# Performance work log

Measured on AMD Instinct MI355X. Metric: run time of the kernel, lower is better.

The kernel has to match this reference:

```python
import jax, jax.numpy as jnp
import numpy as np
from jax import lax

EPS = 1e-5

# sign binarization with straight-through-estimator gradient (identity),
# matching the .data-swap trick in BinarizeConv2d/BinarizeLinear.
@jax.custom_vjp
def ste_sign(x):
    return jnp.sign(x)

def _ste_fwd(x):
    return jnp.sign(x), None

def _ste_bwd(_, g):
    return (g,)

ste_sign.defvjp(_ste_fwd, _ste_bwd)


def conv3x3(x, w):
    # weight is binarized inside the layer; padding=1, stride=1, no bias
    return lax.conv_general_dilated(
        x, ste_sign(w), window_strides=(1, 1), padding=((1, 1), (1, 1)),
        dimension_numbers=('NCHW', 'OIHW', 'NCHW'))


def mp2(x):
    return lax.reduce_window(x, -jnp.inf, lax.max, (1, 1, 2, 2), (1, 1, 2, 2), 'VALID')


def bn2d(x, gamma, beta):
    # training-mode BatchNorm2d: batch statistics over (N, H, W)
    mu = jnp.mean(x, axis=(0, 2, 3), keepdims=True)
    var = jnp.var(x, axis=(0, 2, 3), keepdims=True)
    xn = (x - mu) * lax.rsqrt(var + EPS)
    return xn * gamma[None, :, None, None] + beta[None, :, None, None]


def bn1d(x, gamma=None, beta=None):
    mu = jnp.mean(x, axis=0, keepdims=True)
    var = jnp.var(x, axis=0, keepdims=True)
    xn = (x - mu) * lax.rsqrt(var + EPS)
    if gamma is None:
        return xn
    return xn * gamma[None, :] + beta[None, :]


def hardtanh(x):
    return jnp.clip(x, -1.0, 1.0)


def setup_inputs() -> dict:
    key = jax.random.key(0)
    ks = jax.random.split(key, 16)
    def w(k, shape):
        return jax.random.normal(k, shape, jnp.float32) * 0.1
    d = {'x': jax.random.normal(ks[0], (512, 3, 32, 32), jnp.float32)}
    convs = [(64, 3), (64, 64), (128, 64), (128, 128), (256, 128), (256, 256)]
    for i, (co, ci) in enumerate(convs):
        d[f'w{i+1}'] = w(ks[1 + i], (co, ci, 3, 3))
        d[f'g{i+1}'] = jnp.ones((co,), jnp.float32)
        d[f'b{i+1}'] = jnp.zeros((co,), jnp.float32)
    d['wf1'] = w(ks[7], (512, 256 * 4 * 4))
    d['gf1'] = jnp.ones((512,), jnp.float32)
    d['bf1'] = jnp.zeros((512,), jnp.float32)
    d['wf2'] = w(ks[8], (512, 512))
    d['gf2'] = jnp.ones((512,), jnp.float32)
    d['bf2'] = jnp.zeros((512,), jnp.float32)
    d['wf3'] = w(ks[9], (10, 512))
    return d


def reference(x, w1, g1, b1, w2, g2, b2, w3, g3, b3, w4, g4, b4,
              w5, g5, b5, w6, g6, b6, wf1, gf1, bf1, wf2, gf2, bf2, wf3):
    # block 1: first conv sees raw 3-channel input (not binarized)
    h = hardtanh(bn2d(conv3x3(x, w1), g1, b1))
    h = hardtanh(bn2d(mp2(conv3x3(ste_sign(h), w2)), g2, b2))
    # block 2
    h = hardtanh(bn2d(conv3x3(ste_sign(h), w3), g3, b3))
    h = hardtanh(bn2d(mp2(conv3x3(ste_sign(h), w4)), g4, b4))
    # block 3
    h = hardtanh(bn2d(conv3x3(ste_sign(h), w5), g5, b5))
    h = hardtanh(bn2d(mp2(conv3x3(ste_sign(h), w6)), g6, b6))
    # classifier (all linear inputs binarized: feature dim != 784)
    h = h.reshape(-1, 256 * 4 * 4)
    h = hardtanh(bn1d(ste_sign(h) @ ste_sign(wf1).T, gf1, bf1))
    h = hardtanh(bn1d(ste_sign(h) @ ste_sign(wf2).T, gf2, bf2))
    h = bn1d(ste_sign(h) @ ste_sign(wf3).T)  # affine=False
    return jax.nn.log_softmax(h, axis=-1)
```

## Files before the change

kernel.cpp:

```cpp
#include <hip/hip_runtime.h>
#include <stdint.h>
#include <math.h>


typedef unsigned long long u64;

__device__ __forceinline__ void flag_and_wave(u64* flag, u64 nz) {
    nz &= __shfl_xor(nz, 1);
    nz &= __shfl_xor(nz, 2);
    nz &= __shfl_xor(nz, 4);
    nz &= __shfl_xor(nz, 8);
    nz &= __shfl_xor(nz, 16);
    nz &= __shfl_xor(nz, 32);
    if ((threadIdx.x & 63) == 0) atomicAnd(flag, nz);
}

__global__ void kflag_init(u64* __restrict__ f) {
    int i = threadIdx.x;
    if (i < 16) f[i] = ~0ull;
}

__global__ void kw1t(const float* __restrict__ w1, float* __restrict__ wt) {
    int i = blockIdx.x * 64 + threadIdx.x;
    if (i >= 64 * 27) return;
    int co = i / 27, k = i % 27;
    float v = w1[i];
    wt[k * 64 + co] = (v > 0.f) ? 1.f : ((v < 0.f) ? -1.f : 0.f);
}

__global__ __launch_bounds__(256) void k1_conv_allv(const float* __restrict__ x,
                                                    const float* __restrict__ wt,
                                                    float* __restrict__ out) {
    int gid = blockIdx.x * 256 + threadIdx.x;
    int n = gid >> 8, hw0 = (gid & 255) * 4;
    int y = hw0 >> 5, x0 = hw0 & 31;
    const float* ip = x + (size_t)n * 3 * 1024;
    for (int c0 = 0; c0 < 64; c0 += 16) {
        float4 a[16];
#pragma unroll
        for (int c = 0; c < 16; ++c) a[c] = make_float4(0.f, 0.f, 0.f, 0.f);
        for (int ky = 0; ky < 3; ++ky) {
            int yy = y + ky - 1;
            bool rowok = (unsigned)yy < 32u;
            float win[3][6];
#pragma unroll
            for (int ci = 0; ci < 3; ++ci)
#pragma unroll
                for (int j = 0; j < 6; ++j) {
                    int cc = x0 - 1 + j;
                    bool ok = rowok && ((unsigned)cc < 32u);
                    win[ci][j] = ok ? ip[ci * 1024 + yy * 32 + cc] : 0.f;
                }
#pragma unroll
            for (int kx = 0; kx < 3; ++kx)
#pragma unroll
                for (int ci = 0; ci < 3; ++ci) {
                    const float* wrow = wt + (ci * 9 + ky * 3 + kx) * 64 + c0;
                    float s0 = win[ci][kx], s1 = win[ci][kx + 1];
                    float s2 = win[ci][kx + 2], s3 = win[ci][kx + 3];
#pragma unroll
                    for (int c = 0; c < 16; ++c) {
                        float wv = wrow[c];
                        a[c].x = fmaf(wv, s0, a[c].x);
                        a[c].y = fmaf(wv, s1, a[c].y);
                        a[c].z = fmaf(wv, s2, a[c].z);
                        a[c].w = fmaf(wv, s3, a[c].w);
                    }
                }
        }
#pragma unroll
        for (int c = 0; c < 16; ++c)
            *(float4*)(out + ((size_t)n * 64 + c0 + c) * 1024 + hw0) = a[c];
    }
}

__global__ void k1_statsA(const float* __restrict__ v, double* __restrict__ Sp,
                          double* __restrict__ S2p, int N) {
    int c = blockIdx.x;
    int slot = blockIdx.y * 64 + threadIdx.x;
    double s = 0.0, s2 = 0.0;
    int K = N * 4;
    const float* vp = v + (size_t)c * 1024 + slot;
    int k0 = 0;
    for (; k0 + 32 <= K; k0 += 32) {
        const float* p0 = vp + (size_t)(k0 >> 2) * 65536;
        float buf[32];
#pragma unroll
        for (int j = 0; j < 32; ++j)
            buf[j] = p0[(size_t)(j >> 2) * 65536 + (j & 3) * 256];
#pragma unroll
        for (int j = 0; j < 32; ++j) {
            double t = (double)buf[j];
            s += t; s2 += t * t;
        }
    }
    for (; k0 < K; ++k0) {
        int m = slot + k0 * 256;
        double t = (double)v[((size_t)(m >> 10) * 64 + c) * 1024 + (m & 1023)];
        s += t; s2 += t * t;
    }
    Sp[c * 256 + slot] = s; S2p[c * 256 + slot] = s2;
}

__global__ void k1_statsB(const double* __restrict__ Sp, const double* __restrict__ S2p,
                          float* __restrict__ muF, float* __restrict__ rF, int N) {
    int c = blockIdx.x;
    __shared__ double sh[256], sh2[256];
    sh[threadIdx.x]  = Sp[c * 256 + threadIdx.x];
    sh2[threadIdx.x] = S2p[c * 256 + threadIdx.x];
    __syncthreads();
    for (int o = 128; o > 0; o >>= 1) {
        if ((int)threadIdx.x < o) { sh[threadIdx.x] += sh[threadIdx.x + o]; sh2[threadIdx.x] += sh2[threadIdx.x + o]; }
        __syncthreads();
    }
    if (threadIdx.x == 0) {
        int M = N * 1024;
        double mean = sh[0] / M;
        double var  = sh2[0] / M - mean * mean;
        if (var < 0.0) var = 0.0;
        muF[c] = (float)mean;
        rF[c]  = 1.0f / sqrtf((float)var + 1e-5f);
    }
}

__global__ void k1_signpack(const float* __restrict__ v, const float* __restrict__ muF,
                            const float* __restrict__ rF, const float* __restrict__ g,
                            const float* __restrict__ b, u64* __restrict__ B,
                            u64* __restrict__ NZ, u64* __restrict__ aflag) {
    int gid = blockIdx.x * 64 + threadIdx.x;
    int n = gid >> 8, hw0 = (gid & 255) * 4;
    const float* vp = v + ((size_t)n * 64) * 1024 + hw0;
    u64 bb0 = 0, bb1 = 0, bb2 = 0, bb3 = 0;
    u64 nz0 = 0, nz1 = 0, nz2 = 0, nz3 = 0;
    for (int c0 = 0; c0 < 64; c0 += 16) {
        float4 buf[16];
#pragma unroll
        for (int j = 0; j < 16; ++j)
            buf[j] = *(const float4*)(vp + (size_t)(c0 + j) * 1024);
#pragma unroll
        for (int j = 0; j < 16; ++j) {
            int c = c0 + j;
            float mc = muF[c], rc = rF[c], gc = g[c], bc = b[c];
            float d0 = buf[j].x - mc; float t0 = (d0 * rc) * gc + bc;
            float d1 = buf[j].y - mc; float t1 = (d1 * rc) * gc + bc;
            float d2 = buf[j].z - mc; float t2 = (d2 * rc) * gc + bc;
            float d3 = buf[j].w - mc; float t3 = (d3 * rc) * gc + bc;
            bb0 |= (u64)(t0 > 0.f) << c;  nz0 |= (u64)(t0 != 0.f) << c;
            bb1 |= (u64)(t1 > 0.f) << c;  nz1 |= (u64)(t1 != 0.f) << c;
            bb2 |= (u64)(t2 > 0.f) << c;  nz2 |= (u64)(t2 != 0.f) << c;
            bb3 |= (u64)(t3 > 0.f) << c;  nz3 |= (u64)(t3 != 0.f) << c;
        }
    }
    size_t o = (size_t)n * 1024 + hw0;
    B[o]     = bb0; B[o + 1]  = bb1; B[o + 2]  = bb2; B[o + 3]  = bb3;
    NZ[o]    = nz0; NZ[o + 1] = nz1; NZ[o + 2] = nz2; NZ[o + 3] = nz3;
    flag_and_wave(aflag, nz0 & nz1 & nz2 & nz3);
}

__global__ void k1_conv(const float* __restrict__ x, const float* __restrict__ w1,
                        float* __restrict__ out, int grp) {
    int hw = blockIdx.x * 64 + threadIdx.x;
    int cg = blockIdx.y;
    int n  = blockIdx.z;
    int co = grp * 8 + cg;
    int y = hw >> 5, x0 = hw & 31;
    const float* ip0 = x + ((size_t)n * 3 + 0) * 1024;
    const float* ip1 = x + ((size_t)n * 3 + 1) * 1024;
    const float* ip2 = x + ((size_t)n * 3 + 2) * 1024;
    const float* wp  = w1 + (size_t)co * 27;
    float acc = 0.f;
    for (int ky = 0; ky < 3; ++ky) {
        int yy = y + ky - 1;
        if (yy < 0 || yy > 31) continue;
        for (int kx = 0; kx < 3; ++kx) {
            int xc = x0 + kx - 1;
            if (xc < 0 || xc > 31) continue;
            int sp = yy * 32 + xc;
            int wk = ky * 3 + kx;
            float w0 = wp[wk], w1v = wp[9 + wk], w2 = wp[18 + wk];
            acc += (w0  > 0.f) ? ip0[sp] : ((w0  < 0.f) ? -ip0[sp] : 0.f);
            acc += (w1v > 0.f) ? ip1[sp] : ((w1v < 0.f) ? -ip1[sp] : 0.f);
            acc += (w2  > 0.f) ? ip2[sp] : ((w2  < 0.f) ? -ip2[sp] : 0.f);
        }
    }
    out[((size_t)n * 8 + cg) * 1024 + hw] = acc;
}

__device__ __forceinline__ float ld1(const float* v, int cg, int e) {
    return v[((size_t)(e >> 10) * 8 + cg) * 1024 + (e & 1023)];
}

__global__ void k1_stats(const float* __restrict__ v, float* __restrict__ muF,
                         float* __restrict__ rF, int grp, int N) {
    int cg = blockIdx.x;
    __shared__ double sh[256], sh2[256];
    double s = 0.0, s2 = 0.0;
    int M = N * 1024;
    for (int m = threadIdx.x; m < M; m += 256) {
        double t = (double)ld1(v, cg, m);
        s += t; s2 += t * t;
    }
    sh[threadIdx.x] = s; sh2[threadIdx.x] = s2;
    __syncthreads();
    for (int o = 128; o > 0; o >>= 1) {
        if ((int)threadIdx.x < o) { sh[threadIdx.x] += sh[threadIdx.x + o]; sh2[threadIdx.x] += sh2[threadIdx.x + o]; }
        __syncthreads();
    }
    if (threadIdx.x == 0) {
        double mean = sh[0] / M;
        double var  = sh2[0] / M - mean * mean;
        if (var < 0.0) var = 0.0;
        muF[grp * 8 + cg] = (float)mean;
        rF[grp * 8 + cg]  = 1.0f / sqrtf((float)var + 1e-5f);
    }
}

__global__ void k1_sign(const float* __restrict__ v, const float* __restrict__ muF,
                        const float* __restrict__ rF, const float* __restrict__ g,
                        const float* __restrict__ b, int8_t* __restrict__ sgn, int grp) {
    int hw = blockIdx.x * 256 + threadIdx.x;
    if (hw >= 1024) return;
    int cg = blockIdx.y, n = blockIdx.z;
    int c = grp * 8 + cg;
    float d  = v[((size_t)n * 8 + cg) * 1024 + hw] - muF[c];
    float t  = (d * rF[c]) * g[c] + b[c];
    sgn[((size_t)n * 64 + c) * 1024 + hw] = (int8_t)((t > 0.f) - (t < 0.f));
}

__global__ void kpack_sgn8(const int8_t* __restrict__ s, u64* __restrict__ B,
                           u64* __restrict__ NZ, int C, int HW, u64* __restrict__ aflag) {
    int hw = blockIdx.x * 64 + threadIdx.x;
    int wd = blockIdx.y, n = blockIdx.z;
    int WRD = C >> 6;
    u64 b = 0, nz = ~0ull;
    if (hw < HW) {
        nz = 0;
        const int8_t* sp = s + ((size_t)n * C + wd * 64) * HW + hw;
        for (int j = 0; j < 64; ++j) {
            int v = sp[(size_t)j * HW];
            b  |= (u64)(v > 0) << j;
            nz |= (u64)(v != 0) << j;
        }
        size_t o = ((size_t)n * HW + hw) * WRD + wd;
        B[o] = b; NZ[o] = nz;
    }
    flag_and_wave(aflag, nz);
}

__device__ __forceinline__ void pack_wconv_body(const float* __restrict__ w,
                                                u64* __restrict__ WB, u64* __restrict__ WNZ,
                                                int Ci, int Co, u64* flag, int idx) {
    int WRD = Ci >> 6;
    u64 b = 0, nz = ~0ull;
    if (idx < Co * 9 * WRD) {
        nz = 0;
        int wd = idx % WRD, t = (idx / WRD) % 9, co = idx / (9 * WRD);
        const float* wp = w + ((size_t)co * Ci + wd * 64) * 9 + t;
        float buf[64];
#pragma unroll
        for (int j = 0; j < 64; ++j) buf[j] = wp[(size_t)j * 9];
#pragma unroll
        for (int j = 0; j < 64; ++j) {
            b  |= (u64)(buf[j] > 0.f) << j;
            nz |= (u64)(buf[j] != 0.f) << j;
        }
        WB[idx] = b; WNZ[idx] = nz;
    }
    flag_and_wave(flag, nz);
}

__device__ __forceinline__ void pack_wlinT_body(const float* __restrict__ w,
                                                u64* __restrict__ WBt, u64* __restrict__ WZt,
                                                int K, int O, u64* flag, int idx) {
    int WRD = K >> 6;
    u64 b = 0, nz = ~0ull;
    if (idx < O * WRD) {
        nz = 0;
        int wd = idx % WRD, o = idx / WRD;
        const float* wp = w + (size_t)o * K + wd * 64;
#pragma unroll 8
        for (int j = 0; j < 64; ++j) {
            float v = wp[j];
            b  |= (u64)(v > 0.f) << j;
            nz |= (u64)(v != 0.f) << j;
        }
        WBt[(size_t)wd * O + o] = b; WZt[(size_t)wd * O + o] = nz;
    }
    flag_and_wave(flag, nz);
}

__global__ void kpack_all(const float* __restrict__ w2, const float* __restrict__ w3,
                          const float* __restrict__ w4, const float* __restrict__ w5,
                          const float* __restrict__ w6, const float* __restrict__ wf1,
                          const float* __restrict__ wf2, const float* __restrict__ wf3,
                          u64* wb2B, u64* wb2Z, u64* wb3B, u64* wb3Z,
                          u64* wb4B, u64* wb4Z, u64* wb5B, u64* wb5Z,
                          u64* wb6B, u64* wb6Z, u64* wf1B, u64* wf1Z,
                          u64* wf2B, u64* wf2Z, u64* wf3B, u64* wf3Z,
                          u64* flags) {
    int b = blockIdx.x, t = threadIdx.x;
    if      (b <   3) pack_wconv_body(w2, wb2B, wb2Z,  64,  64, &flags[0], b * 256 + t);
    else if (b <   8) pack_wconv_body(w3, wb3B, wb3Z,  64, 128, &flags[1], (b - 3) * 256 + t);
    else if (b <  17) pack_wconv_body(w4, wb4B, wb4Z, 128, 128, &flags[2], (b - 8) * 256 + t);
    else if (b <  35) pack_wconv_body(w5, wb5B, wb5Z, 128, 256, &flags[3], (b - 17) * 256 + t);
    else if (b <  71) pack_wconv_body(w6, wb6B, wb6Z, 256, 256, &flags[4], (b - 35) * 256 + t);
    else if (b < 199) pack_wlinT_body(wf1, wf1B, wf1Z, 4096, 512, &flags[5], (b - 71) * 256 + t);
    else if (b < 215) pack_wlinT_body(wf2, wf2B, wf2Z,  512, 512, &flags[6], (b - 199) * 256 + t);
    else              pack_wlinT_body(wf3, wf3B, wf3Z,  512,  10, &flags[7], (b - 215) * 256 + t);
}

template <int WRD, int CB>
__device__ __forceinline__ void conv_slow(const u64* __restrict__ ib, const u64* __restrict__ iz,
                                          const u64* __restrict__ wbp, const u64* __restrict__ wzp,
                                          int H, int Wi, int y, int x, int* acc) {
#pragma unroll
    for (int c = 0; c < CB; ++c) acc[c] = 0;
    for (int ky = 0; ky < 3; ++ky) {
        int yy = y + ky - 1;
        if ((unsigned)yy >= (unsigned)H) continue;
        for (int kx = 0; kx < 3; ++kx) {
            int xc = x + kx - 1;
            if ((unsigned)xc >= (unsigned)Wi) continue;
            int p = yy * Wi + xc, t = ky * 3 + kx;
            u64 xb[WRD], xz[WRD];
#pragma unroll
            for (int w = 0; w < WRD; ++w) {
                xb[w] = ib[(size_t)p * WRD + w];
                xz[w] = iz[(size_t)p * WRD + w];
            }
#pragma unroll
            for (int c = 0; c < CB; ++c) {
#pragma unroll
                for (int w = 0; w < WRD; ++w) {
                    u64 e = xz[w] & wzp[(c * 9 + t) * WRD + w];
                    acc[c] += __popcll(e) - 2 * __popcll((xb[w] ^ wbp[(c * 9 + t) * WRD + w]) & e);
                }
            }
        }
    }
}

template <int WRD, int CB>
__device__ __forceinline__ void conv_fast(const u64* __restrict__ ib,
                                          const u64* __restrict__ wbp,
                                          int H, int Wi, int y, int x, int* acc) {
    int a2[CB];
#pragma unroll
    for (int c = 0; c < CB; ++c) a2[c] = 0;
    int T = 0;
    for (int ky = 0; ky < 3; ++ky) {
        int yy = y + ky - 1;
        if ((unsigned)yy >= (unsigned)H) continue;
        for (int kx = 0; kx < 3; ++kx) {
            int xc = x + kx - 1;
            if ((unsigned)xc >= (unsigned)Wi) continue;
            int p = yy * Wi + xc, t = ky * 3 + kx;
            ++T;
            u64 xb[WRD];
#pragma unroll
            for (int w = 0; w < WRD; ++w) xb[w] = ib[(size_t)p * WRD + w];
#pragma unroll
            for (int c = 0; c < CB; ++c)
#pragma unroll
                for (int w = 0; w < WRD; ++w)
                    a2[c] += __popcll(xb[w] ^ wbp[(c * 9 + t) * WRD + w]);
        }
    }
#pragma unroll
    for (int c = 0; c < CB; ++c) acc[c] = 64 * WRD * T - 2 * a2[c];
}

template <int WRD, int CB>
__global__ void kbconv2(const u64* __restrict__ B, const u64* __restrict__ NZ,
                        const u64* __restrict__ WB, const u64* __restrict__ WNZ,
                        int16_t* __restrict__ out, int Co, int H, int Wi,
                        const u64* __restrict__ wflag, const u64* __restrict__ aflag) {
    int hw = blockIdx.x * 64 + threadIdx.x;
    if (hw >= H * Wi) return;
    int co0 = blockIdx.y * CB, n = blockIdx.z;
    int y = hw / Wi, x = hw % Wi;
    const u64* ib = B  + (size_t)n * H * Wi * WRD;
    const u64* iz = NZ + (size_t)n * H * Wi * WRD;
    const u64* wbp = WB  + (size_t)co0 * 9 * WRD;
    const u64* wzp = WNZ + (size_t)co0 * 9 * WRD;
    bool fast = ((*wflag) & (*aflag)) == ~0ull;
    int acc[CB];
    if (fast) conv_fast<WRD, CB>(ib, wbp, H, Wi, y, x, acc);
    else      conv_slow<WRD, CB>(ib, iz, wbp, wzp, H, Wi, y, x, acc);
#pragma unroll
    for (int c = 0; c < CB; ++c)
        out[((size_t)n * Co + co0 + c) * H * Wi + hw] = (int16_t)acc[c];
}

template <int WRD, int CB>
__global__ void kbconv_pool2(const u64* __restrict__ B, const u64* __restrict__ NZ,
                             const u64* __restrict__ WB, const u64* __restrict__ WNZ,
                             int16_t* __restrict__ out, int Co, int H, int Wi,
                             const u64* __restrict__ wflag, const u64* __restrict__ aflag) {
    int Ho = H >> 1, Wo = Wi >> 1;
    int hw = blockIdx.x * 64 + threadIdx.x;
    if (hw >= Ho * Wo) return;
    int co0 = blockIdx.y * CB, n = blockIdx.z;
    int yo = hw / Wo, xo = hw % Wo;
    const u64* ib = B  + (size_t)n * H * Wi * WRD;
    const u64* iz = NZ + (size_t)n * H * Wi * WRD;
    const u64* wbp = WB  + (size_t)co0 * 9 * WRD;
    const u64* wzp = WNZ + (size_t)co0 * 9 * WRD;
    bool fast = ((*wflag) & (*aflag)) == ~0ull;
    int best[CB];
#pragma unroll
    for (int c = 0; c < CB; ++c) best[c] = -(1 << 30);
    if (fast) {
        for (int dy = 0; dy < 2; ++dy)
            for (int dx = 0; dx < 2; ++dx) {
                int acc[CB];
                conv_fast<WRD, CB>(ib, wbp, H, Wi, 2 * yo + dy, 2 * xo + dx, acc);
#pragma unroll
                for (int c = 0; c < CB; ++c) best[c] = acc[c] > best[c] ? acc[c] : best[c];
            }
    } else {
        for (int dy = 0; dy < 2; ++dy)
            for (int dx = 0; dx < 2; ++dx) {
                int acc[CB];
                conv_slow<WRD, CB>(ib, iz, wbp, wzp, H, Wi, 2 * yo + dy, 2 * xo + dx, acc);
#pragma unroll
                for (int c = 0; c < CB; ++c) best[c] = acc[c] > best[c] ? acc[c] : best[c];
            }
    }
#pragma unroll
    for (int c = 0; c < CB; ++c)
        out[((size_t)n * Co + co0 + c) * Ho * Wo + hw] = (int16_t)best[c];
}

template <int WRD, int CB>
__global__ void kbconv_pool2s(const u64* __restrict__ B, const u64* __restrict__ NZ,
                              const u64* __restrict__ WB, const u64* __restrict__ WNZ,
                              int16_t* __restrict__ out, int Co, int H, int Wi,
                              const u64* __restrict__ wflag, const u64* __restrict__ aflag) {
    int Ho = H >> 1, Wo = Wi >> 1;
    int t0 = threadIdx.x;
    int pix = t0 & 15, pos = t0 >> 4;
    int co0 = blockIdx.y * CB, n = blockIdx.z;
    int yo = pix / Wo, xo = pix % Wo;
    int y = 2 * yo + (pos >> 1), x = 2 * xo + (pos & 1);
    const u64* ib = B  + (size_t)n * H * Wi * WRD;
    const u64* iz = NZ + (size_t)n * H * Wi * WRD;
    const u64* wbp = WB  + (size_t)co0 * 9 * WRD;
    const u64* wzp = WNZ + (size_t)co0 * 9 * WRD;
    bool fast = ((*wflag) & (*aflag)) == ~0ull;
    int acc[CB];
    if (fast) conv_fast<WRD, CB>(ib, wbp, H, Wi, y, x, acc);
    else      conv_slow<WRD, CB>(ib, iz, wbp, wzp, H, Wi, y, x, acc);
#pragma unroll
    for (int c = 0; c < CB; ++c) {
        int v = acc[c];
        int v1 = __shfl_xor(v, 16); v = v1 > v ? v1 : v;
        int v2 = __shfl_xor(v, 32); v = v2 > v ? v2 : v;
        acc[c] = v;
    }
    if (pos == 0) {
#pragma unroll
        for (int c = 0; c < CB; ++c)
            out[((size_t)n * Co + co0 + c) * Ho * Wo + pix] = (int16_t)acc[c];
    }
}

__global__ void kaccum16(const int16_t* __restrict__ v, long long* __restrict__ Sp,
                         long long* __restrict__ S2p, int C, int HW, int M) {
    int c = blockIdx.x;
    long long s = 0, s2 = 0;
    int M8 = M >> 3;
    for (int g = blockIdx.y * 256 + threadIdx.x; g < M8; g += gridDim.y * 256) {
        int m0 = g * 8;
        const int16_t* p = v + ((size_t)(m0 / HW) * C + c) * HW + (m0 % HW);
        short4 a = *(const short4*)p;
        short4 b = *(const short4*)(p + 4);
        int v0 = a.x, v1 = a.y, v2 = a.z, v3 = a.w;
        int v4 = b.x, v5 = b.y, v6 = b.z, v7 = b.w;
        s  += v0 + v1 + v2 + v3 + v4 + v5 + v6 + v7;
        s2 += (long long)v0 * v0 + (long long)v1 * v1 + (long long)v2 * v2 + (long long)v3 * v3
            + (long long)v4 * v4 + (long long)v5 * v5 + (long long)v6 * v6 + (long long)v7 * v7;
    }
    __shared__ long long sh[256], sh2[256];
    sh[threadIdx.x] = s; sh2[threadIdx.x] = s2;
    __syncthreads();
    for (int o = 128; o > 0; o >>= 1) {
        if ((int)threadIdx.x < o) { sh[threadIdx.x] += sh[threadIdx.x + o]; sh2[threadIdx.x] += sh2[threadIdx.x + o]; }
        __syncthreads();
    }
    if (threadIdx.x == 0) {
        Sp[c * gridDim.y + blockIdx.y]  = sh[0];
        S2p[c * gridDim.y + blockIdx.y] = sh2[0];
    }
}

__global__ void kfinal2(const long long* __restrict__ Sp, const long long* __restrict__ S2p,
                        int NB, const float* __restrict__ g, const float* __restrict__ b,
                        double* __restrict__ mu, double* __restrict__ Ad,
                        double* __restrict__ Bd, int C, int M) {
    int c = blockIdx.x * 64 + threadIdx.x;
    if (c >= C) return;
    long long s = 0, s2 = 0;
    for (int i = 0; i < NB; ++i) { s += Sp[c * NB + i]; s2 += S2p[c * NB + i]; }
    double mean = (double)s / M;
    double var  = (double)s2 / M - mean * mean;
    if (var < 0.0) var = 0.0;
    mu[c] = mean;
    Ad[c] = (g ? (double)g[c] : 1.0) / sqrt(var + 1e-5);
    Bd[c] = b ? (double)b[c] : 0.0;
}

__global__ void ksp_conv(const int16_t* __restrict__ v, const double* __restrict__ mu,
                         const double* __restrict__ Ad, const double* __restrict__ Bd,
                         u64* __restrict__ B, u64* __restrict__ NZ, int C, int HW, int N,
                         u64* __restrict__ aflag) {
    int tid = blockIdx.x * 64 + threadIdx.x;
    int WRD = C >> 6;
    int HW4 = HW >> 2;
    int total = N * WRD * HW4;
    u64 nzall = ~0ull;
    if (tid < total) {
        int hw4 = tid % HW4;
        int wd  = (tid / HW4) % WRD;
        int n   = tid / (HW4 * WRD);
        const int16_t* vp = v + ((size_t)n * C + wd * 64) * HW + hw4 * 4;
        u64 b0 = 0, b1 = 0, b2 = 0, b3 = 0;
        u64 n0 = 0, n1 = 0, n2 = 0, n3 = 0;
        for (int j0 = 0; j0 < 64; j0 += 16) {
            short4 buf[16];
#pragma unroll
            for (int j = 0; j < 16; ++j)
                buf[j] = *(const short4*)(vp + (size_t)(j0 + j) * HW);
#pragma unroll
            for (int j = 0; j < 16; ++j) {
                int c = wd * 64 + j0 + j;
                double Mu = mu[c], A = Ad[c], Bb = Bd[c];
                double t0 = ((double)buf[j].x - Mu) * A + Bb;
                double t1 = ((double)buf[j].y - Mu) * A + Bb;
                double t2 = ((double)buf[j].z - Mu) * A + Bb;
                double t3 = ((double)buf[j].w - Mu) * A + Bb;
                int sh = j0 + j;
                b0 |= (u64)(t0 > 0.0) << sh;  n0 |= (u64)(t0 != 0.0) << sh;
                b1 |= (u64)(t1 > 0.0) << sh;  n1 |= (u64)(t1 != 0.0) << sh;
                b2 |= (u64)(t2 > 0.0) << sh;  n2 |= (u64)(t2 != 0.0) << sh;
                b3 |= (u64)(t3 > 0.0) << sh;  n3 |= (u64)(t3 != 0.0) << sh;
            }
        }
        size_t o = ((size_t)n * HW + hw4 * 4) * WRD + wd;
        B[o] = b0;  B[o + WRD] = b1;  B[o + 2 * WRD] = b2;  B[o + 3 * WRD] = b3;
        NZ[o] = n0; NZ[o + WRD] = n1; NZ[o + 2 * WRD] = n2; NZ[o + 3 * WRD] = n3;
        nzall = n0 & n1 & n2 & n3;
    }
    flag_and_wave(aflag, nzall);
}

__global__ void ksp_flat(const int16_t* __restrict__ v, const double* __restrict__ mu,
                         const double* __restrict__ Ad, const double* __restrict__ Bd,
                         u64* __restrict__ B, u64* __restrict__ NZ, u64* __restrict__ aflag) {
    int wd = threadIdx.x;
    int n  = blockIdx.x;
    const int16_t* vp = v + (size_t)n * 4096 + wd * 64;
    int16_t buf[64];
#pragma unroll
    for (int j = 0; j < 64; ++j) buf[j] = vp[j];
    u64 b = 0, nz = 0;
#pragma unroll
    for (int j = 0; j < 64; ++j) {
        int k = wd * 64 + j;
        int c = k >> 4;
        double t = ((double)buf[j] - mu[c]) * Ad[c] + Bd[c];
        b  |= (u64)(t > 0.0) << j;
        nz |= (u64)(t != 0.0) << j;
    }
    B[(size_t)n * 64 + wd] = b; NZ[(size_t)n * 64 + wd] = nz;
    flag_and_wave(aflag, nz);
}

__global__ void ksp_fc(const int* __restrict__ v, const double* __restrict__ mu,
                       const double* __restrict__ Ad, const double* __restrict__ Bd,
                       u64* __restrict__ B, u64* __restrict__ NZ, int C, int WRD, int N,
                       u64* __restrict__ aflag) {
    int tid = blockIdx.x * 64 + threadIdx.x;
    u64 nz = ~0ull;
    if (tid < N * WRD) {
        int n = tid / WRD, wd = tid % WRD;
        const int* vp = v + (size_t)n * C + wd * 64;
        int buf[64];
#pragma unroll
        for (int j = 0; j < 64; ++j) buf[j] = vp[j];
        u64 b = 0; nz = 0;
#pragma unroll
        for (int j = 0; j < 64; ++j) {
            int c = wd * 64 + j;
            double t = ((double)buf[j] - mu[c]) * Ad[c] + Bd[c];
            b  |= (u64)(t > 0.0) << j;
            nz |= (u64)(t != 0.0) << j;
        }
        B[(size_t)n * WRD + wd] = b; NZ[(size_t)n * WRD + wd] = nz;
    }
    flag_and_wave(aflag, nz);
}

__global__ void kbfc(const u64* __restrict__ aB, const u64* __restrict__ aNZ,
                     const u64* __restrict__ wBt, const u64* __restrict__ wZt,
                     int* __restrict__ out, int WRD, int O,
                     const u64* __restrict__ wflag, const u64* __restrict__ aflag) {
    int o = blockIdx.x * 64 + threadIdx.x;
    if (o >= O) return;
    int n = blockIdx.y;
    const u64* ab = aB  + (size_t)n * WRD;
    const u64* az = aNZ + (size_t)n * WRD;
    bool fast = ((*wflag) & (*aflag)) == ~0ull;
    int acc;
    if (fast) {
        int a2 = 0;
        for (int w = 0; w < WRD; w += 8) {
            u64 aw[8], ww[8];
#pragma unroll
            for (int j = 0; j < 8; ++j) {
                aw[j] = ab[w + j];
                ww[j] = wBt[(size_t)(w + j) * O + o];
            }
#pragma unroll
            for (int j = 0; j < 8; ++j) a2 += __popcll(aw[j] ^ ww[j]);
        }
        acc = 64 * WRD - 2 * a2;
    } else {
        acc = 0;
        for (int w = 0; w < WRD; ++w) {
            u64 wb = wBt[(size_t)w * O + o];
            u64 wz = wZt[(size_t)w * O + o];
            u64 e = az[w] & wz;
            acc += __popcll(e) - 2 * __popcll((ab[w] ^ wb) & e);
        }
    }
    out[(size_t)n * O + o] = acc;
}

__global__ void k3_stats(const int* __restrict__ v, int N, int C,
                         const float* __restrict__ g, const float* __restrict__ b,
                         double* __restrict__ mu, double* __restrict__ Ad,
                         double* __restrict__ Bd) {
    int c = blockIdx.x;
    __shared__ double sh[256], sh2[256];
    double s = 0.0, s2 = 0.0;
    for (int n = threadIdx.x; n < N; n += 256) {
        double t = (double)v[(size_t)n * C + c];
        s += t; s2 += t * t;
    }
    sh[threadIdx.x] = s; sh2[threadIdx.x] = s2;
    __syncthreads();
    for (int o = 128; o > 0; o >>= 1) {
        if ((int)threadIdx.x < o) { sh[threadIdx.x] += sh[threadIdx.x + o]; sh2[threadIdx.x] += sh2[threadIdx.x + o]; }
        __syncthreads();
    }
    if (threadIdx.x == 0) {
        double mean = sh[0] / N;
        double var  = sh2[0] / N - mean * mean;
        if (var < 0.0) var = 0.0;
        mu[c] = mean;
        Ad[c] = (g ? (double)g[c] : 1.0) / sqrt(var + 1e-5);
        Bd[c] = b ? (double)b[c] : 0.0;
    }
}

__global__ void k4_out(const int* __restrict__ v, const double* __restrict__ mu,
                       const double* __restrict__ Ad, float* __restrict__ out, int N) {
    int n = blockIdx.x * 256 + threadIdx.x;
    if (n >= N) return;
    double z[10];
    double mx = -1e300;
    for (int o = 0; o < 10; ++o) {
        z[o] = ((double)v[n * 10 + o] - mu[o]) * Ad[o];
        if (z[o] > mx) mx = z[o];
    }
    double s = 0.0;
    for (int o = 0; o < 10; ++o) s += exp(z[o] - mx);
    double l = mx + log(s);
    for (int o = 0; o < 10; ++o) out[n * 10 + o] = (float)(z[o] - l);
}

extern "C" void kernel_launch(void* const* d_in, const int* in_sizes, int n_in,
                              void* d_out, int out_size, void* d_ws, size_t ws_size,
                              hipStream_t stream) {
    const int N = in_sizes[0] / (3 * 32 * 32);

    const float* x   = (const float*)d_in[0];
    const float* w1  = (const float*)d_in[1];
    const float* g1  = (const float*)d_in[2];
    const float* b1  = (const float*)d_in[3];
    const float* w2  = (const float*)d_in[4];
    const float* g2  = (const float*)d_in[5];
    const float* b2  = (const float*)d_in[6];
    const float* w3  = (const float*)d_in[7];
    const float* g3  = (const float*)d_in[8];
    const float* b3  = (const float*)d_in[9];
    const float* w4  = (const float*)d_in[10];
    const float* g4  = (const float*)d_in[11];
    const float* b4  = (const float*)d_in[12];
    const float* w5  = (const float*)d_in[13];
    const float* g5  = (const float*)d_in[14];
    const float* b5  = (const float*)d_in[15];
    const float* w6  = (const float*)d_in[16];
    const float* g6  = (const float*)d_in[17];
    const float* b6  = (const float*)d_in[18];
    const float* wf1 = (const float*)d_in[19];
    const float* gf1 = (const float*)d_in[20];
    const float* bf1 = (const float*)d_in[21];
    const float* wf2 = (const float*)d_in[22];
    const float* gf2 = (const float*)d_in[23];
    const float* bf2 = (const float*)d_in[24];
    const float* wf3 = (const float*)d_in[25];

    char* ws = (char*)d_ws;
    size_t off = 0;
    auto alloc = [&](size_t bytes) -> char* {
        char* p = ws + off;
        off = (off + bytes + 511) & ~(size_t)511;
        return p;
    };

    int16_t* t2  = (int16_t*)alloc((size_t)N * 64 * 256 * 2);
    u64* p2B = (u64*)alloc((size_t)N * 256 * 8);
    u64* p2Z = (u64*)alloc((size_t)N * 256 * 8);
    int16_t* t3  = (int16_t*)alloc((size_t)N * 128 * 256 * 2);
    u64* p3B = (u64*)alloc((size_t)N * 256 * 2 * 8);
    u64* p3Z = (u64*)alloc((size_t)N * 256 * 2 * 8);
    int16_t* t4  = (int16_t*)alloc((size_t)N * 128 * 64 * 2);
    u64* p4B = (u64*)alloc((size_t)N * 64 * 2 * 8);
    u64* p4Z = (u64*)alloc((size_t)N * 64 * 2 * 8);
    int16_t* t5  = (int16_t*)alloc((size_t)N * 256 * 64 * 2);
    u64* p5B = (u64*)alloc((size_t)N * 64 * 4 * 8);
    u64* p5Z = (u64*)alloc((size_t)N * 64 * 4 * 8);
    int16_t* t6  = (int16_t*)alloc((size_t)N * 256 * 16 * 2);
    u64* p6B = (u64*)alloc((size_t)N * 64 * 8);
    u64* p6Z = (u64*)alloc((size_t)N * 64 * 8);
    int* fc1 = (int*)alloc((size_t)N * 512 * 4);
    int* fc2 = (int*)alloc((size_t)N * 512 * 4);
    int* fc3 = (int*)alloc((size_t)N * 10 * 4);
    u64* pF1B = (u64*)alloc((size_t)N * 8 * 8);
    u64* pF1Z = (u64*)alloc((size_t)N * 8 * 8);
    u64* pF2B = (u64*)alloc((size_t)N * 8 * 8);
    u64* pF2Z = (u64*)alloc((size_t)N * 8 * 8);
    size_t down_end = off;

    size_t head_big = (size_t)N * 64 * 1024 * 4;
    bool big = ws_size >= head_big + ((size_t)20 << 20);
    float*  c1buf = (float*)ws;
    float*  c1buf8 = (float*)ws;
    int8_t* sgnA  = (int8_t*)(ws + (size_t)N * 8 * 1024 * 4);

    off = big ? (head_big > down_end ? head_big : down_end) : down_end;
    off = (off + 511) & ~(size_t)511;
    u64* p1B = (u64*)alloc((size_t)N * 1024 * 8);
    u64* p1Z = (u64*)alloc((size_t)N * 1024 * 8);
    u64* wb2B = (u64*)alloc(64  * 9 * 1 * 8);  u64* wb2Z = (u64*)alloc(64  * 9 * 1 * 8);
    u64* wb3B = (u64*)alloc(128 * 9 * 1 * 8);  u64* wb3Z = (u64*)alloc(128 * 9 * 1 * 8);
    u64* wb4B = (u64*)alloc(128 * 9 * 2 * 8);  u64* wb4Z = (u64*)alloc(128 * 9 * 2 * 8);
    u64* wb5B = (u64*)alloc(256 * 9 * 2 * 8);  u64* wb5Z = (u64*)alloc(256 * 9 * 2 * 8);
    u64* wb6B = (u64*)alloc(256 * 9 * 4 * 8);  u64* wb6Z = (u64*)alloc(256 * 9 * 4 * 8);
    u64* wf1B = (u64*)alloc(512 * 64 * 8);     u64* wf1Z = (u64*)alloc(512 * 64 * 8);
    u64* wf2B = (u64*)alloc(512 * 8 * 8);      u64* wf2Z = (u64*)alloc(512 * 8 * 8);
    u64* wf3B = (u64*)alloc(10 * 8 * 8);       u64* wf3Z = (u64*)alloc(10 * 8 * 8);
    float* wt = (float*)alloc(27 * 64 * 4);
    double* Sp  = (double*)alloc(64 * 256 * 8);
    double* S2p = (double*)alloc(64 * 256 * 8);
    long long* SpI  = (long long*)alloc(256 * 32 * 8);
    long long* S2pI = (long long*)alloc(256 * 32 * 8);
    u64* flags = (u64*)alloc(16 * 8);
    double* mu = (double*)alloc(512 * 8);
    double* Ad = (double*)alloc(512 * 8);
    double* Bd = (double*)alloc(512 * 8);
    float*  muF = (float*)alloc(64 * 4);
    float*  rF  = (float*)alloc(64 * 4);

    auto cdiv = [](int a, int b) { return (a + b - 1) / b; };

    kflag_init<<<1, 64, 0, stream>>>(flags);
    kpack_all<<<216, 256, 0, stream>>>(w2, w3, w4, w5, w6, wf1, wf2, wf3,
                                       wb2B, wb2Z, wb3B, wb3Z, wb4B, wb4Z,
                                       wb5B, wb5Z, wb6B, wb6Z, wf1B, wf1Z,
                                       wf2B, wf2Z, wf3B, wf3Z, flags);

    if (big) {
        kw1t<<<27, 64, 0, stream>>>(w1, wt);
        k1_conv_allv<<<(N * 256) / 256, 256, 0, stream>>>(x, wt, c1buf);
        k1_statsA<<<dim3(64, 4), 64, 0, stream>>>(c1buf, Sp, S2p, N);
        k1_statsB<<<64, 256, 0, stream>>>(Sp, S2p, muF, rF, N);
        k1_signpack<<<(N * 256) / 64, 64, 0, stream>>>(c1buf, muF, rF, g1, b1, p1B, p1Z, &flags[8]);
    } else {
        for (int grp = 0; grp < 8; ++grp) {
            k1_conv<<<dim3(16, 8, N), 64, 0, stream>>>(x, w1, c1buf8, grp);
            k1_stats<<<8, 256, 0, stream>>>(c1buf8, muF, rF, grp, N);
            k1_sign<<<dim3(4, 8, N), 256, 0, stream>>>(c1buf8, muF, rF, g1, b1, sgnA, grp);
        }
        kpack_sgn8<<<dim3(16, 1, N), 64, 0, stream>>>(sgnA, p1B, p1Z, 64, 1024, &flags[8]);
    }

    kbconv_pool2<1, 8><<<dim3(4, 8, N), 64, 0, stream>>>(p1B, p1Z, wb2B, wb2Z, t2, 64, 32, 32, &flags[0], &flags[8]);
    kaccum16<<<dim3(64, 32), 256, 0, stream>>>(t2, SpI, S2pI, 64, 256, N * 256);
    kfinal2<<<1, 64, 0, stream>>>(SpI, S2pI, 32, g2, b2, mu, Ad, Bd, 64, N * 256);
    ksp_conv<<<cdiv(N * 1 * 64, 64), 64, 0, stream>>>(t2, mu, Ad, Bd, p2B, p2Z, 64, 256, N, &flags[9]);

    kbconv2<1, 8><<<dim3(4, 16, N), 64, 0, stream>>>(p2B, p2Z, wb3B, wb3Z, t3, 128, 16, 16, &flags[1], &flags[9]);
    kaccum16<<<dim3(128, 16), 256, 0, stream>>>(t3, SpI, S2pI, 128, 256, N * 256);
    kfinal2<<<2, 64, 0, stream>>>(SpI, S2pI, 16, g3, b3, mu, Ad, Bd, 128, N * 256);
    ksp_conv<<<cdiv(N * 2 * 64, 64), 64, 0, stream>>>(t3, mu, Ad, Bd, p3B, p3Z, 128, 256, N, &flags[10]);

    kbconv_pool2<2, 8><<<dim3(1, 16, N), 64, 0, stream>>>(p3B, p3Z, wb4B, wb4Z, t4, 128, 16, 16, &flags[2], &flags[10]);
    kaccum16<<<dim3(128, 16), 256, 0, stream>>>(t4, SpI, S2pI, 128, 64, N * 64);
    kfinal2<<<2, 64, 0, stream>>>(SpI, S2pI, 16, g4, b4, mu, Ad, Bd, 128, N * 64);
    ksp_conv<<<cdiv(N * 2 * 16, 64), 64, 0, stream>>>(t4, mu, Ad, Bd, p4B, p4Z, 128, 64, N, &flags[11]);

    kbconv2<2, 8><<<dim3(1, 32, N), 64, 0, stream>>>(p4B, p4Z, wb5B, wb5Z, t5, 256, 8, 8, &flags[3], &flags[11]);
    kaccum16<<<dim3(256, 8), 256, 0, stream>>>(t5, SpI, S2pI, 256, 64, N * 64);
    kfinal2<<<4, 64, 0, stream>>>(SpI, S2pI, 8, g5, b5, mu, Ad, Bd, 256, N * 64);
    ksp_conv<<<cdiv(N * 4 * 16, 64), 64, 0, stream>>>(t5, mu, Ad, Bd, p5B, p5Z, 256, 64, N, &flags[12]);

    kbconv_pool2s<4, 8><<<dim3(1, 32, N), 64, 0, stream>>>(p5B, p5Z, wb6B, wb6Z, t6, 256, 8, 8, &flags[4], &flags[12]);
    kaccum16<<<dim3(256, 2), 256, 0, stream>>>(t6, SpI, S2pI, 256, 16, N * 16);
    kfinal2<<<4, 64, 0, stream>>>(SpI, S2pI, 2, g6, b6, mu, Ad, Bd, 256, N * 16);
    ksp_flat<<<N, 64, 0, stream>>>(t6, mu, Ad, Bd, p6B, p6Z, &flags[13]);

    kbfc<<<dim3(8, N), 64, 0, stream>>>(p6B, p6Z, wf1B, wf1Z, fc1, 64, 512, &flags[5], &flags[13]);
    k3_stats<<<512, 256, 0, stream>>>(fc1, N, 512, gf1, bf1, mu, Ad, Bd);
    ksp_fc<<<cdiv(N * 8, 64), 64, 0, stream>>>(fc1, mu, Ad, Bd, pF1B, pF1Z, 512, 8, N, &flags[14]);

    kbfc<<<dim3(8, N), 64, 0, stream>>>(pF1B, pF1Z, wf2B, wf2Z, fc2, 8, 512, &flags[6], &flags[14]);
    k3_stats<<<512, 256, 0, stream>>>(fc2, N, 512, gf2, bf2, mu, Ad, Bd);
    ksp_fc<<<cdiv(N * 8, 64), 64, 0, stream>>>(fc2, mu, Ad, Bd, pF2B, pF2Z, 512, 8, N, &flags[15]);

    kbfc<<<dim3(1, N), 64, 0, stream>>>(pF2B, pF2Z, wf3B, wf3Z, fc3, 8, 10, &flags[7], &flags[15]);
    k3_stats<<<10, 256, 0, stream>>>(fc3, N, 10, nullptr, nullptr, mu, Ad, Bd);
    k4_out<<<cdiv(N, 256), 256, 0, stream>>>(fc3, mu, Ad, (float*)d_out, N);
}
```

Measured before the change: 642.6 us.

## Fuse BN finalize into sign-pack kernels and split first conv over channel halves

Result: no change. 648.3 us (+0.9%).

```diff
diff --git a/kernel.cpp b/kernel.cpp
--- a/kernel.cpp
+++ b/kernel.cpp
@@ -28,14 +28,16 @@
     wt[k * 64 + co] = (v > 0.f) ? 1.f : ((v < 0.f) ? -1.f : 0.f);
 }
 
-__global__ __launch_bounds__(256) void k1_conv_allv(const float* __restrict__ x,
-                                                    const float* __restrict__ wt,
-                                                    float* __restrict__ out) {
+__global__ __launch_bounds__(256) void k1_conv_allv2(const float* __restrict__ x,
+                                                     const float* __restrict__ wt,
+                                                     float* __restrict__ out) {
     int gid = blockIdx.x * 256 + threadIdx.x;
     int n = gid >> 8, hw0 = (gid & 255) * 4;
+    int cbase = blockIdx.y * 32;
     int y = hw0 >> 5, x0 = hw0 & 31;
     const float* ip = x + (size_t)n * 3 * 1024;
-    for (int c0 = 0; c0 < 64; c0 += 16) {
+    for (int cc = 0; cc < 32; cc += 16) {
+        int c0 = cbase + cc;
         float4 a[16];
 #pragma unroll
         for (int c = 0; c < 16; ++c) a[c] = make_float4(0.f, 0.f, 0.f, 0.f);
@@ -47,9 +49,9 @@
             for (int ci = 0; ci < 3; ++ci)
 #pragma unroll
                 for (int j = 0; j < 6; ++j) {
-                    int cc = x0 - 1 + j;
-                    bool ok = rowok && ((unsigned)cc < 32u);
-                    win[ci][j] = ok ? ip[ci * 1024 + yy * 32 + cc] : 0.f;
+                    int ccx = x0 - 1 + j;
+                    bool ok = rowok && ((unsigned)ccx < 32u);
+                    win[ci][j] = ok ? ip[ci * 1024 + yy * 32 + ccx] : 0.f;
                 }
 #pragma unroll
             for (int kx = 0; kx < 3; ++kx)
@@ -494,26 +496,23 @@
     }
 }
 
-__global__ void kfinal2(const long long* __restrict__ Sp, const long long* __restrict__ S2p,
-                        int NB, const float* __restrict__ g, const float* __restrict__ b,
-                        double* __restrict__ mu, double* __restrict__ Ad,
-                        double* __restrict__ Bd, int C, int M) {
-    int c = blockIdx.x * 64 + threadIdx.x;
-    if (c >= C) return;
-    long long s = 0, s2 = 0;
-    for (int i = 0; i < NB; ++i) { s += Sp[c * NB + i]; s2 += S2p[c * NB + i]; }
-    double mean = (double)s / M;
-    double var  = (double)s2 / M - mean * mean;
-    if (var < 0.0) var = 0.0;
-    mu[c] = mean;
-    Ad[c] = (g ? (double)g[c] : 1.0) / sqrt(var + 1e-5);
-    Bd[c] = b ? (double)b[c] : 0.0;
-}
-
-__global__ void ksp_conv(const int16_t* __restrict__ v, const double* __restrict__ mu,
-                         const double* __restrict__ Ad, const double* __restrict__ Bd,
-                         u64* __restrict__ B, u64* __restrict__ NZ, int C, int HW, int N,
-                         u64* __restrict__ aflag) {
+__global__ void ksp_conv2(const int16_t* __restrict__ v,
+                          const long long* __restrict__ Sp, const long long* __restrict__ S2p,
+                          int NB, const float* __restrict__ g, const float* __restrict__ b,
+                          u64* __restrict__ B, u64* __restrict__ NZ, int C, int HW, int N,
+                          int M, u64* __restrict__ aflag) {
+    __shared__ double sMu[256], sA[256], sB[256];
+    for (int c = threadIdx.x; c < C; c += 64) {
+        long long s = 0, s2 = 0;
+        for (int i = 0; i < NB; ++i) { s += Sp[c * NB + i]; s2 += S2p[c * NB + i]; }
+        double mean = (double)s / M;
+        double var  = (double)s2 / M - mean * mean;
+        if (var < 0.0) var = 0.0;
+        sMu[c] = mean;
+        sA[c]  = (g ? (double)g[c] : 1.0) / sqrt(var + 1e-5);
+        sB[c]  = b ? (double)b[c] : 0.0;
+    }
+    __syncthreads();
     int tid = blockIdx.x * 64 + threadIdx.x;
     int WRD = C >> 6;
     int HW4 = HW >> 2;
@@ -534,7 +533,7 @@
 #pragma unroll
             for (int j = 0; j < 16; ++j) {
                 int c = wd * 64 + j0 + j;
-                double Mu = mu[c], A = Ad[c], Bb = Bd[c];
+                double Mu = sMu[c], A = sA[c], Bb = sB[c];
                 double t0 = ((double)buf[j].x - Mu) * A + Bb;
                 double t1 = ((double)buf[j].y - Mu) * A + Bb;
                 double t2 = ((double)buf[j].z - Mu) * A + Bb;
@@ -554,25 +553,39 @@
     flag_and_wave(aflag, nzall);
 }
 
-__global__ void ksp_flat(const int16_t* __restrict__ v, const double* __restrict__ mu,
-                         const double* __restrict__ Ad, const double* __restrict__ Bd,
-                         u64* __restrict__ B, u64* __restrict__ NZ, u64* __restrict__ aflag) {
+__global__ void ksp_flat2(const int16_t* __restrict__ v,
+                          const long long* __restrict__ Sp, const long long* __restrict__ S2p,
+                          int NB, const float* __restrict__ g, const float* __restrict__ b,
+                          u64* __restrict__ B, u64* __restrict__ NZ, int M,
+                          u64* __restrict__ aflag) {
+    __shared__ double sMu[256], sA[256], sB[256];
+    for (int c = threadIdx.x; c < 256; c += 64) {
+        long long s = 0, s2 = 0;
+        for (int i = 0; i < NB; ++i) { s += Sp[c * NB + i]; s2 += S2p[c * NB + i]; }
+        double mean = (double)s / M;
+        double var  = (double)s2 / M - mean * mean;
+        if (var < 0.0) var = 0.0;
+        sMu[c] = mean;
+        sA[c]  = (g ? (double)g[c] : 1.0) / sqrt(var + 1e-5);
+        sB[c]  = b ? (double)b[c] : 0.0;
+    }
+    __syncthreads();
     int wd = threadIdx.x;
     int n  = blockIdx.x;
     const int16_t* vp = v + (size_t)n * 4096 + wd * 64;
     int16_t buf[64];
 #pragma unroll
     for (int j = 0; j < 64; ++j) buf[j] = vp[j];
-    u64 b = 0, nz = 0;
+    u64 b2 = 0, nz = 0;
 #pragma unroll
     for (int j = 0; j < 64; ++j) {
         int k = wd * 64 + j;
         int c = k >> 4;
-        double t = ((double)buf[j] - mu[c]) * Ad[c] + Bd[c];
-        b  |= (u64)(t > 0.0) << j;
+        double t = ((double)buf[j] - sMu[c]) * sA[c] + sB[c];
+        b2 |= (u64)(t > 0.0) << j;
         nz |= (u64)(t != 0.0) << j;
     }
-    B[(size_t)n * 64 + wd] = b; NZ[(size_t)n * 64 + wd] = nz;
+    B[(size_t)n * 64 + wd] = b2; NZ[(size_t)n * 64 + wd] = nz;
     flag_and_wave(aflag, nz);
 }
 
@@ -784,7 +797,7 @@
 
     if (big) {
         kw1t<<<27, 64, 0, stream>>>(w1, wt);
-        k1_conv_allv<<<(N * 256) / 256, 256, 0, stream>>>(x, wt, c1buf);
+        k1_conv_allv2<<<dim3((N * 256) / 256, 2), 256, 0, stream>>>(x, wt, c1buf);
         k1_statsA<<<dim3(64, 4), 64, 0, stream>>>(c1buf, Sp, S2p, N);
         k1_statsB<<<64, 256, 0, stream>>>(Sp, S2p, muF, rF, N);
         k1_signpack<<<(N * 256) / 64, 64, 0, stream>>>(c1buf, muF, rF, g1, b1, p1B, p1Z, &flags[8]);
@@ -799,28 +812,23 @@
 
     kbconv_pool2<1, 8><<<dim3(4, 8, N), 64, 0, stream>>>(p1B, p1Z, wb2B, wb2Z, t2, 64, 32, 32, &flags[0], &flags[8]);
     kaccum16<<<dim3(64, 32), 256, 0, stream>>>(t2, SpI, S2pI, 64, 256, N * 256);
-    kfinal2<<<1, 64, 0, stream>>>(SpI, S2pI, 32, g2, b2, mu, Ad, Bd, 64, N * 256);
-    ksp_conv<<<cdiv(N * 1 * 64, 64), 64, 0, stream>>>(t2, mu, Ad, Bd, p2B, p2Z, 64, 256, N, &flags[9]);
+    ksp_conv2<<<cdiv(N * 1 * 64, 64), 64, 0, stream>>>(t2, SpI, S2pI, 32, g2, b2, p2B, p2Z, 64, 256, N, N * 256, &flags[9]);
 
     kbconv2<1, 8><<<dim3(4, 16, N), 64, 0, stream>>>(p2B, p2Z, wb3B, wb3Z, t3, 128, 16, 16, &flags[1], &flags[9]);
     kaccum16<<<dim3(128, 16), 256, 0, stream>>>(t3, SpI, S2pI, 128, 256, N * 256);
-    kfinal2<<<2, 64, 0, stream>>>(SpI, S2pI, 16, g3, b3, mu, Ad, Bd, 128, N * 256);
-    ksp_conv<<<cdiv(N * 2 * 64, 64), 64, 0, stream>>>(t3, mu, Ad, Bd, p3B, p3Z, 128, 256, N, &flags[10]);
+    ksp_conv2<<<cdiv(N * 2 * 64, 64), 64, 0, stream>>>(t3, SpI, S2pI, 16, g3, b3, p3B, p3Z, 128, 256, N, N * 256, &flags[10]);
 
     kbconv_pool2<2, 8><<<dim3(1, 16, N), 64, 0, stream>>>(p3B, p3Z, wb4B, wb4Z, t4, 128, 16, 16, &flags[2], &flags[10]);
     kaccum16<<<dim3(128, 16), 256, 0, stream>>>(t4, SpI, S2pI, 128, 64, N * 64);
-    kfinal2<<<2, 64, 0, stream>>>(SpI, S2pI, 16, g4, b4, mu, Ad, Bd, 128, N * 64);
-    ksp_conv<<<cdiv(N * 2 * 16, 64), 64, 0, stream>>>(t4, mu, Ad, Bd, p4B, p4Z, 128, 64, N, &flags[11]);
+    ksp_conv2<<<cdiv(N * 2 * 16, 64), 64, 0, stream>>>(t4, SpI, S2pI, 16, g4, b4, p4B, p4Z, 128, 64, N, N * 64, &flags[11]);
 
     kbconv2<2, 8><<<dim3(1, 32, N), 64, 0, stream>>>(p4B, p4Z, wb5B, wb5Z, t5, 256, 8, 8, &flags[3], &flags[11]);
     kaccum16<<<dim3(256, 8), 256, 0, stream>>>(t5, SpI, S2pI, 256, 64, N * 64);
-    kfinal2<<<4, 64, 0, stream>>>(SpI, S2pI, 8, g5, b5, mu, Ad, Bd, 256, N * 64);
-    ksp_conv<<<cdiv(N * 4 * 16, 64), 64, 0, stream>>>(t5, mu, Ad, Bd, p5B, p5Z, 256, 64, N, &flags[12]);
+    ksp_conv2<<<cdiv(N * 4 * 16, 64), 64, 0, stream>>>(t5, SpI, S2pI, 8, g5, b5, p5B, p5Z, 256, 64, N, N * 64, &flags[12]);
 
     kbconv_pool2s<4, 8><<<dim3(1, 32, N), 64, 0, stream>>>(p5B, p5Z, wb6B, wb6Z, t6, 256, 8, 8, &flags[4], &flags[12]);
     kaccum16<<<dim3(256, 2), 256, 0, stream>>>(t6, SpI, S2pI, 256, 16, N * 16);
-    kfinal2<<<4, 64, 0, stream>>>(SpI, S2pI, 2, g6, b6, mu, Ad, Bd, 256, N * 16);
-    ksp_flat<<<N, 64, 0, stream>>>(t6, mu, Ad, Bd, p6B, p6Z, &flags[13]);
+    ksp_flat2<<<N, 64, 0, stream>>>(t6, SpI, S2pI, 2, g6, b6, p6B, p6Z, N * 16, &flags[13]);
 
     kbfc<<<dim3(8, N), 64, 0, stream>>>(p6B, p6Z, wf1B, wf1Z, fc1, 64, 512, &flags[5], &flags[13]);
     k3_stats<<<512, 256, 0, stream>>>(fc1, N, 512, gf1, bf1, mu, Ad, Bd);
```
